# Kernel optimization log

Measured on AMD Instinct MI355X. Metric: run time of the kernel, lower is better.

## Reference

```python
import jax, jax.numpy as jnp
import numpy as np

SR = 16000.0          # sample_rate
T = 262144            # audio_length
MAX_OL = 2.0          # max oscillator level
N_FRAMES = 250        # ADSR envelope frame grid
TWO_PI = 2.0 * np.pi
EPS = 1e-5


def adsr_env(floor, peak, attack, decay, sus, release):
    """Differentiable ADSR envelope on a fixed N_FRAMES grid. Params: [B]."""
    f = lambda x: x[:, None]
    floor, peak, a, d, s, r = map(f, (floor, peak, attack, decay, sus, release))
    a = jnp.maximum(a, EPS)
    d = jnp.maximum(d, EPS)
    r = jnp.maximum(r, EPS)
    t = jnp.linspace(0.0, 1.0, N_FRAMES, dtype=jnp.float32)  # [F]
    att = jnp.clip(t / a, 0.0, 1.0)
    dec = jnp.clip((t - a) / d, 0.0, 1.0)
    rel = jnp.clip((t - (1.0 - r)) / r, 0.0, 1.0)
    env = att * (1.0 - (1.0 - s) * dec) * (1.0 - rel)  # [B, F]
    return floor + (peak - floor) * env


def resample_frames(env, n):
    """Linear-interp resample [B, N_FRAMES] -> [B, n]."""
    pos = jnp.linspace(0.0, N_FRAMES - 1.0, n, dtype=jnp.float32)
    i0 = jnp.floor(pos).astype(jnp.int32)
    i1 = jnp.minimum(i0 + 1, N_FRAMES - 1)
    frac = pos - i0.astype(jnp.float32)
    return env[:, i0] * (1.0 - frac) + env[:, i1] * frac


def setup_inputs() -> dict:
    key = jax.random.key(0)
    k1, k2, k3, k4 = jax.random.split(key, 4)
    return {
        "mod_index": jax.random.normal(k1, (32, 6), dtype=jnp.float32),
        "freq_ratio": jax.random.uniform(k2, (32, 6), dtype=jnp.float32),
        "f0": jax.random.uniform(k3, (32, T), dtype=jnp.float32),
        "adsr": jax.random.uniform(k4, (32, 11), dtype=jnp.float32),
    }


def reference(mod_index, freq_ratio, f0, adsr):
    mi = MAX_OL * jax.nn.sigmoid(mod_index)          # scaled mod index [B,6]
    omega = jnp.cumsum(TWO_PI * f0 / SR, axis=1)     # instantaneous phase [B,T]

    def op(k, mod):
        # k is 0-based operator index (OP1=0 .. OP6=5); mod is [B,T] or 0.
        phase = freq_ratio[:, k:k + 1] * omega + TWO_PI * mod
        out = mi[:, k:k + 1] * jnp.sin(phase % TWO_PI)
        env = adsr_env(adsr[:, 0 + k], adsr[:, 1 + k], adsr[:, 2 + k],
                       adsr[:, 3 + k], adsr[:, 4 + k], adsr[:, 5 + k])
        env = resample_frames(env, out.shape[1])
        return out * env

    op6 = op(5, 0.0)
    op5 = op(4, op6)
    op4 = op(3, op5)
    op3 = op(2, op4)
    op2 = op(1, 0.0)
    op1 = op(0, op2)
    return (op3 + op1) / MAX_OL
```

## Files before the change

kernel.cpp:

```cpp
#include <hip/hip_runtime.h>
#include <math.h>

#define B 32
#define T 262144
#define NFR 250
#define NCH 64
#define CHUNK 4096
#define NTHR 256
#define EPT 16

#define STEPF (249.0f / 262143.0f)

typedef float v2f __attribute__((ext_vector_type(2)));

__device__ __forceinline__ int swz16(int t, int e) {
  return t * 16 + (e ^ ((t & 3) << 2));
}

__global__ __launch_bounds__(NTHR) void k_partial(const float* __restrict__ f0,
                                                  double* __restrict__ partials) {
  int row = blockIdx.y, ch = blockIdx.x, t = threadIdx.x;
  const float4* p = (const float4*)(f0 + (size_t)row * T + ch * CHUNK);
  double s = 0.0;
#pragma unroll
  for (int i = 0; i < CHUNK / 4 / NTHR; ++i) {
    float4 v = p[i * NTHR + t];
    s += (double)v.x + (double)v.y + (double)v.z + (double)v.w;
  }
#pragma unroll
  for (int d = 32; d > 0; d >>= 1) s += __shfl_down(s, d);
  __shared__ double wsum[NTHR / 64];
  int lane = t & 63, wid = t >> 6;
  if (lane == 0) wsum[wid] = s;
  __syncthreads();
  if (t == 0) {
    double tot = 0.0;
#pragma unroll
    for (int w = 0; w < NTHR / 64; ++w) tot += wsum[w];
    __hip_atomic_store(&partials[row * NCH + ch], tot, __ATOMIC_RELAXED,
                       __HIP_MEMORY_SCOPE_AGENT);
  }
}

__global__ __launch_bounds__(NTHR, 6) void k_main(const float* __restrict__ f0,
                                                  const float* __restrict__ mod_index,
                                                  const float* __restrict__ freq_ratio,
                                                  const float* __restrict__ adsr,
                                                  const double* __restrict__ partials,
                                                  float* __restrict__ out) {
  __shared__ __align__(16) float tile[NTHR * EPT];
  __shared__ double wsum[NTHR / 64];
  __shared__ float envtab[8][6];
  __shared__ float emsh[6];

  int row = blockIdx.y, ch = blockIdx.x, t = threadIdx.x;
  int lane = t & 63, wid = t >> 6;
  size_t rowOff = (size_t)row * T;

  const float4* fp4 = (const float4*)(f0 + rowOff + ch * CHUNK + t * EPT);
  float4 v4[4];
#pragma unroll
  for (int q = 0; q < 4; ++q) v4[q] = fp4[q];

  double pv = 0.0;
  if (lane < ch)
    pv = __hip_atomic_load(&partials[row * NCH + lane], __ATOMIC_RELAXED,
                           __HIP_MEMORY_SCOPE_AGENT);
#pragma unroll
  for (int d = 32; d > 0; d >>= 1) pv += __shfl_down(pv, d);
  double cbase = __shfl(pv, 0);

  int i0_blk = ch * CHUNK;
  int i0s_blk = (int)floorf((float)i0_blk * STEPF);
  if (t < 48) {
    int fr = t / 6, k = t - 6 * fr;
    int fi = i0s_blk + fr;
    fi = (fi < NFR - 1) ? fi : NFR - 1;
    const float* ap = adsr + row * 11 + k;
    float fl = ap[0], pk = ap[1];
    float a = fmaxf(ap[2], 1e-5f);
    float de = fmaxf(ap[3], 1e-5f);
    float ss = ap[4];
    float r = fmaxf(ap[5], 1e-5f);
    float tt = (float)fi * (1.0f / 249.0f);
    float att = fminf(fmaxf(tt / a, 0.0f), 1.0f);
    float dec = fminf(fmaxf((tt - a) / de, 0.0f), 1.0f);
    float rel = fminf(fmaxf((tt - (1.0f - r)) / r, 0.0f), 1.0f);
    float env = att * (1.0f - (1.0f - ss) * dec) * (1.0f - rel);
    envtab[fr][k] = fl + (pk - fl) * env;
  } else if (t < 54) {
    int k = t - 48;
    float em = 2.0f / (1.0f + expf(-mod_index[row * 6 + k]));
    emsh[k] = (k == 0 || k == 2) ? 0.5f * em : em;
  }

  float sv[EPT];
  {
    float a = 0.0f;
#pragma unroll
    for (int q = 0; q < 4; ++q) {
      a += v4[q].x; sv[4 * q] = a;
      a += v4[q].y; sv[4 * q + 1] = a;
      a += v4[q].z; sv[4 * q + 2] = a;
      a += v4[q].w; sv[4 * q + 3] = a;
    }
  }
  double ts = (double)sv[EPT - 1];

  double x = ts;
#pragma unroll
  for (int d = 1; d < 64; d <<= 1) {
    double n = __shfl_up(x, d);
    if (lane >= d) x += n;
  }
  if (lane == 63) wsum[wid] = x;
  __syncthreads();
  double wbase = 0.0;
#pragma unroll
  for (int w = 0; w < NTHR / 64; ++w) wbase += (w < wid) ? wsum[w] : 0.0;
  float sbase = (float)(cbase + wbase + (x - ts));

#pragma unroll
  for (int e = 0; e < EPT; ++e) sv[e] += sbase;

  int i0 = ch * CHUNK + t * EPT;
  int i0s = (int)floorf((float)i0 * STEPF);
  float pr0 = (float)i0 * STEPF - (float)i0s;
  int idx = i0s - i0s_blk;

  float frs[6], c0[6], s0[6], dd6[6];
#pragma unroll
  for (int k = 0; k < 6; ++k) {
    frs[k] = freq_ratio[row * 6 + k] * (1.0f / 16000.0f);
    float em = emsh[k];
    float E0 = envtab[idx][k], E1 = envtab[idx + 1][k], E2 = envtab[idx + 2][k];
    c0[k] = E0 * em;
    s0[k] = (E1 - E0) * em;
    dd6[k] = (E2 - E1) * em - s0[k];
  }

  auto sin2 = [](v2f x) -> v2f {
    return (v2f){__builtin_amdgcn_sinf(__builtin_amdgcn_fractf(x.x)),
                 __builtin_amdgcn_sinf(__builtin_amdgcn_fractf(x.y))};
  };

#pragma unroll
  for (int h = 0; h < 2; ++h) {
    const int b0 = h * 8;
    v2f sv2[4], pr2[4], m2[4], o2[4];
#pragma unroll
    for (int p = 0; p < 4; ++p) {
      sv2[p] = (v2f){sv[b0 + 2 * p], sv[b0 + 2 * p + 1]};
      v2f pr = (v2f){pr0 + (float)(b0 + 2 * p) * STEPF,
                     pr0 + (float)(b0 + 2 * p + 1) * STEPF};
      pr2[p] = pr;
      m2[p] = __builtin_elementwise_max(pr - (v2f){1.0f, 1.0f},
                                        (v2f){0.0f, 0.0f});
    }
    auto env2 = [&](int k, int p) -> v2f {
      return __builtin_elementwise_fma(
          m2[p], (v2f){dd6[k], dd6[k]},
          __builtin_elementwise_fma(pr2[p], (v2f){s0[k], s0[k]},
                                    (v2f){c0[k], c0[k]}));
    };
#pragma unroll
    for (int p = 0; p < 4; ++p)
      o2[p] = sin2((v2f){frs[5], frs[5]} * sv2[p]) * env2(5, p);
#pragma unroll
    for (int p = 0; p < 4; ++p)
      o2[p] = sin2(__builtin_elementwise_fma((v2f){frs[4], frs[4]}, sv2[p], o2[p])) * env2(4, p);
#pragma unroll
    for (int p = 0; p < 4; ++p)
      o2[p] = sin2(__builtin_elementwise_fma((v2f){frs[3], frs[3]}, sv2[p], o2[p])) * env2(3, p);
#pragma unroll
    for (int p = 0; p < 4; ++p)
      o2[p] = sin2(__builtin_elementwise_fma((v2f){frs[2], frs[2]}, sv2[p], o2[p])) * env2(2, p);
#pragma unroll
    for (int p = 0; p < 4; ++p) {
      v2f q2 = sin2((v2f){frs[1], frs[1]} * sv2[p]) * env2(1, p);
      v2f q1 = sin2(__builtin_elementwise_fma((v2f){frs[0], frs[0]}, sv2[p], q2)) * env2(0, p);
      o2[p] += q1;
    }
    float4 ov;
    ov.x = o2[0].x; ov.y = o2[0].y; ov.z = o2[1].x; ov.w = o2[1].y;
    *(float4*)&tile[swz16(t, b0)] = ov;
    ov.x = o2[2].x; ov.y = o2[2].y; ov.z = o2[3].x; ov.w = o2[3].y;
    *(float4*)&tile[swz16(t, b0 + 4)] = ov;
  }
  __syncthreads();

  float4* ob = (float4*)(out + rowOff + ch * CHUNK);
#pragma unroll
  for (int i = 0; i < 4; ++i) {
    int li = i * 1024 + t * 4;
    int tt = li >> 4, ee = li & 15;
    ob[i * NTHR + t] = *(const float4*)&tile[swz16(tt, ee)];
  }
}

extern "C" void kernel_launch(void* const* d_in, const int* in_sizes, int n_in,
                              void* d_out, int out_size, void* d_ws, size_t ws_size,
                              hipStream_t stream) {
  const float* mod_index  = (const float*)d_in[0];
  const float* freq_ratio = (const float*)d_in[1];
  const float* f0         = (const float*)d_in[2];
  const float* adsr       = (const float*)d_in[3];
  float* out = (float*)d_out;

  double* partials = (double*)d_ws;

  hipLaunchKernelGGL(k_partial, dim3(NCH, B), dim3(NTHR), 0, stream, f0, partials);
  hipLaunchKernelGGL(k_main, dim3(NCH, B), dim3(NTHR), 0, stream,
                     f0, mod_index, freq_ratio, adsr, partials, out);
}
```

Measured before the change: 27.39 us.

## Fuse partial-sum and main kernels via chained scan with dynamic block ordering

Replaces the two-kernel approach (a separate pass that reduces f0 chunk partials, then the main kernel) with a single kernel. It takes a dynamic ticket from an atomic counter so blocks are ordered by chunk, publishes each block's chunk sum to a padded slot, and spin-waits on earlier chunks' sums to form the row prefix. This removes the second full read of f0 and one kernel launch. In exchange it adds a memset of the workspace, atomic polling latency, and a serial dependency chain across chunks. Summing predecessors is parallel across lanes, so only publish-to-consume latency is serialized.

New measurement: 48.47 us. 1.77x slower.

```diff
diff --git a/kernel.cpp b/kernel.cpp
--- a/kernel.cpp
+++ b/kernel.cpp
@@ -8,8 +8,12 @@
 #define CHUNK 4096
 #define NTHR 256
 #define EPT 16
+#define NBLK (B * NCH)
 
 #define STEPF (249.0f / 262143.0f)
+
+#define VSTRIDE 32
+#define WS_CLEAR (NBLK * 256 + 256)
 
 typedef float v2f __attribute__((ext_vector_type(2)));
 
@@ -17,58 +21,31 @@
   return t * 16 + (e ^ ((t & 3) << 2));
 }
 
-__global__ __launch_bounds__(NTHR) void k_partial(const float* __restrict__ f0,
-                                                  double* __restrict__ partials) {
-  int row = blockIdx.y, ch = blockIdx.x, t = threadIdx.x;
-  const float4* p = (const float4*)(f0 + (size_t)row * T + ch * CHUNK);
-  double s = 0.0;
-#pragma unroll
-  for (int i = 0; i < CHUNK / 4 / NTHR; ++i) {
-    float4 v = p[i * NTHR + t];
-    s += (double)v.x + (double)v.y + (double)v.z + (double)v.w;
-  }
-#pragma unroll
-  for (int d = 32; d > 0; d >>= 1) s += __shfl_down(s, d);
-  __shared__ double wsum[NTHR / 64];
-  int lane = t & 63, wid = t >> 6;
-  if (lane == 0) wsum[wid] = s;
-  __syncthreads();
-  if (t == 0) {
-    double tot = 0.0;
-#pragma unroll
-    for (int w = 0; w < NTHR / 64; ++w) tot += wsum[w];
-    __hip_atomic_store(&partials[row * NCH + ch], tot, __ATOMIC_RELAXED,
-                       __HIP_MEMORY_SCOPE_AGENT);
-  }
-}
-
-__global__ __launch_bounds__(NTHR, 6) void k_main(const float* __restrict__ f0,
-                                                  const float* __restrict__ mod_index,
-                                                  const float* __restrict__ freq_ratio,
-                                                  const float* __restrict__ adsr,
-                                                  const double* __restrict__ partials,
-                                                  float* __restrict__ out) {
+__global__ __launch_bounds__(NTHR, 6) void k_one(
+    const float* __restrict__ f0, const float* __restrict__ mod_index,
+    const float* __restrict__ freq_ratio, const float* __restrict__ adsr,
+    unsigned long long* __restrict__ vals, unsigned int* __restrict__ counter,
+    float* __restrict__ out) {
   __shared__ __align__(16) float tile[NTHR * EPT];
   __shared__ double wsum[NTHR / 64];
+  __shared__ double cbsh;
+  __shared__ int stk;
   __shared__ float envtab[8][6];
   __shared__ float emsh[6];
 
-  int row = blockIdx.y, ch = blockIdx.x, t = threadIdx.x;
-  int lane = t & 63, wid = t >> 6;
+  int t = threadIdx.x, lane = t & 63, wid = t >> 6;
+
+  if (t == 0) stk = (int)atomicAdd(counter, 1u);
+  __syncthreads();
+  int tk = stk;
+  int ch = tk >> 5;
+  int row = tk & 31;
   size_t rowOff = (size_t)row * T;
 
   const float4* fp4 = (const float4*)(f0 + rowOff + ch * CHUNK + t * EPT);
   float4 v4[4];
 #pragma unroll
   for (int q = 0; q < 4; ++q) v4[q] = fp4[q];
-
-  double pv = 0.0;
-  if (lane < ch)
-    pv = __hip_atomic_load(&partials[row * NCH + lane], __ATOMIC_RELAXED,
-                           __HIP_MEMORY_SCOPE_AGENT);
-#pragma unroll
-  for (int d = 32; d > 0; d >>= 1) pv += __shfl_down(pv, d);
-  double cbase = __shfl(pv, 0);
 
   int i0_blk = ch * CHUNK;
   int i0s_blk = (int)floorf((float)i0_blk * STEPF);
@@ -115,11 +92,35 @@
   }
   if (lane == 63) wsum[wid] = x;
   __syncthreads();
-  double wbase = 0.0;
-#pragma unroll
-  for (int w = 0; w < NTHR / 64; ++w) wbase += (w < wid) ? wsum[w] : 0.0;
-  float sbase = (float)(cbase + wbase + (x - ts));
-
+  double wbase = 0.0, tot = 0.0;
+#pragma unroll
+  for (int w = 0; w < NTHR / 64; ++w) {
+    double s = wsum[w];
+    wbase += (w < wid) ? s : 0.0;
+    tot += s;
+  }
+
+  if (t == 0)
+    atomicExch(vals + (size_t)tk * VSTRIDE,
+               (unsigned long long)__double_as_longlong(tot));
+
+  if (wid == 0) {
+    double pv = 0.0;
+    if (lane < ch) {
+      unsigned long long* slot =
+          vals + (size_t)((lane << 5) + row) * VSTRIDE;
+      unsigned long long bits;
+      while ((bits = atomicAdd(slot, 0ULL)) == 0ULL)
+        __builtin_amdgcn_s_sleep(8);
+      pv = __longlong_as_double((long long)bits);
+    }
+#pragma unroll
+    for (int d = 32; d > 0; d >>= 1) pv += __shfl_down(pv, d);
+    if (lane == 0) cbsh = pv;
+  }
+  __syncthreads();
+
+  float sbase = (float)(cbsh + wbase + (x - ts));
 #pragma unroll
   for (int e = 0; e < EPT; ++e) sv[e] += sbase;
 
@@ -139,9 +140,9 @@
     dd6[k] = (E2 - E1) * em - s0[k];
   }
 
-  auto sin2 = [](v2f x) -> v2f {
-    return (v2f){__builtin_amdgcn_sinf(__builtin_amdgcn_fractf(x.x)),
-                 __builtin_amdgcn_sinf(__builtin_amdgcn_fractf(x.y))};
+  auto sin2 = [](v2f x2) -> v2f {
+    return (v2f){__builtin_amdgcn_sinf(__builtin_amdgcn_fractf(x2.x)),
+                 __builtin_amdgcn_sinf(__builtin_amdgcn_fractf(x2.y))};
   };
 
 #pragma unroll
@@ -207,9 +208,11 @@
   const float* adsr       = (const float*)d_in[3];
   float* out = (float*)d_out;
 
-  double* partials = (double*)d_ws;
-
-  hipLaunchKernelGGL(k_partial, dim3(NCH, B), dim3(NTHR), 0, stream, f0, partials);
-  hipLaunchKernelGGL(k_main, dim3(NCH, B), dim3(NTHR), 0, stream,
-                     f0, mod_index, freq_ratio, adsr, partials, out);
+  char* ws = (char*)d_ws;
+  unsigned long long* vals = (unsigned long long*)ws;
+  unsigned int* counter = (unsigned int*)(ws + NBLK * 256);
+
+  hipMemsetAsync(ws, 0, WS_CLEAR, stream);
+  hipLaunchKernelGGL(k_one, dim3(NBLK), dim3(NTHR), 0, stream,
+                     f0, mod_index, freq_ratio, adsr, vals, counter, out);
 }
```
